# Kernel tuning notes

Measured on AMD Instinct MI355X. Metric: run time of the kernel, lower is better.

## Reference

```python
import jax, jax.numpy as jnp
import numpy as np

NUM_HEADS = 16
ROPE_THETA = 10000.0


def _rope_cos_sin(head_dim, seq_len, theta=ROPE_THETA):
    # matches precompute_freqs_cis: theta ** (-(2i)/head_dim)
    exps = -(jnp.arange(0, head_dim, 2)[: head_dim // 2].astype(jnp.float32)) / head_dim
    freqs = theta ** exps                                   # [hd/2]
    ang = jnp.arange(seq_len, dtype=jnp.float32)[:, None] * freqs[None, :]  # [S, hd/2]
    return jnp.cos(ang), jnp.sin(ang)


def _apply_rope(x, cos, sin):
    # x: [B, H, S, hd]; interpret consecutive pairs as complex numbers
    x2 = x.reshape(*x.shape[:-1], -1, 2)
    xr, xi = x2[..., 0], x2[..., 1]
    c = cos[None, None]  # [1,1,S,hd/2]
    s = sin[None, None]
    outr = xr * c - xi * s
    outi = xr * s + xi * c
    return jnp.stack([outr, outi], axis=-1).reshape(x.shape)


def setup_inputs() -> dict:
    key = jax.random.key(0)
    ks = jax.random.split(key, 9)
    B, S, D = 2, 2048, 1024
    scale = 0.02
    x = jax.random.normal(ks[0], (B, S, D), jnp.float32)
    Wq = jax.random.normal(ks[1], (D, D), jnp.float32) * scale
    bq = jax.random.normal(ks[2], (D,), jnp.float32) * scale
    Wk = jax.random.normal(ks[3], (D, D), jnp.float32) * scale
    bk = jax.random.normal(ks[4], (D,), jnp.float32) * scale
    Wv = jax.random.normal(ks[5], (D, D), jnp.float32) * scale
    bv = jax.random.normal(ks[6], (D,), jnp.float32) * scale
    Wo = jax.random.normal(ks[7], (D, D), jnp.float32) * scale
    return {"x": x, "Wq": Wq, "bq": bq, "Wk": Wk, "bk": bk,
            "Wv": Wv, "bv": bv, "Wo": Wo}


def reference(x, Wq, bq, Wk, bk, Wv, bv, Wo):
    B, S, D = x.shape
    H = NUM_HEADS
    hd = D // H
    # projections (torch Linear: x @ W.T + b), split heads -> [B,H,S,hd]
    q = (x @ Wq.T + bq).reshape(B, S, H, hd).transpose(0, 2, 1, 3)
    k = (x @ Wk.T + bk).reshape(B, S, H, hd).transpose(0, 2, 1, 3)
    v = (x @ Wv.T + bv).reshape(B, S, H, hd).transpose(0, 2, 1, 3)
    cos, sin = _rope_cos_sin(hd, S)
    q = _apply_rope(q, cos, sin)
    k = _apply_rope(k, cos, sin)
    # NOTE: original scales by sqrt(input_dim), not sqrt(head_dim)
    inv_scale = 1.0 / jnp.sqrt(jnp.asarray(D, jnp.float32))
    scores = jax.nn.softmax(jnp.einsum('bhqd,bhkd->bhqk', q, k) * inv_scale, axis=-1)
    out = jnp.einsum('bhqk,bhkd->bhqd', scores, v)
    out = out.transpose(0, 2, 1, 3).reshape(B, S, D)
    return out @ Wo.T
```

## Files before the change

### kernel.cpp

```cpp
#include <hip/hip_runtime.h>
#include <math.h>

namespace {
constexpr int kB = 2;
constexpr int kS = 2048;
constexpr int kD = 1024;
constexpr int kH = 16;
constexpr int kHD = 64;
constexpr int kBS = kB * kS;
constexpr float kInvScale = 0.03125f;
constexpr int BM = 128, BN = 64, BK = 64;
}

typedef __attribute__((ext_vector_type(8))) short short8;
typedef __attribute__((ext_vector_type(4))) float f32x4;
typedef __attribute__((ext_vector_type(4))) unsigned short u16x4;
typedef __attribute__((ext_vector_type(4))) unsigned int u32x4;

__device__ inline unsigned short f2bf(float f) {
  union { float f; unsigned u; } v;
  v.f = f;
  unsigned r = v.u + 0x7FFFu + ((v.u >> 16) & 1u);
  return (unsigned short)(r >> 16);
}

__device__ inline unsigned pack_bf16_pair(float lo, float hi) {
  union { float f; unsigned u; } a, b;
  a.f = hi; b.f = lo;
  return __builtin_amdgcn_perm(a.u + 0x8000u, b.u + 0x8000u, 0x07060302u);
}

__device__ inline void gload_lds16(const unsigned short* g, unsigned short* l) {
  __builtin_amdgcn_global_load_lds(
      (const __attribute__((address_space(1))) void*)g,
      (__attribute__((address_space(3))) void*)l, 16, 0, 0);
}

__global__ __launch_bounds__(256) void cast_prep_kernel(
    const float* __restrict__ x, const float* __restrict__ Wq,
    const float* __restrict__ Wk, const float* __restrict__ Wv,
    const float* __restrict__ Wo, unsigned short* __restrict__ xb,
    unsigned short* __restrict__ wb, float2* __restrict__ rope) {
  const int tid = blockIdx.x * 256 + threadIdx.x;
  const int stride = gridDim.x * 256;
  for (int i = tid; i < 1048576; i += stride) {
    const float* src;
    unsigned short* dst;
    int off;
    if (i < 524288) {
      src = x; dst = xb; off = i;
    } else {
      const int j = i - 524288;
      const int w = j >> 17;
      src = (w == 0) ? Wq : (w == 1) ? Wk : (w == 2) ? Wv : Wo;
      dst = wb + (size_t)w * (kD * kD);
      off = j & 131071;
    }
    const float4 a = reinterpret_cast<const float4*>(src)[off * 2];
    const float4 b = reinterpret_cast<const float4*>(src)[off * 2 + 1];
    short8 o;
    o[0] = (short)f2bf(a.x); o[1] = (short)f2bf(a.y);
    o[2] = (short)f2bf(a.z); o[3] = (short)f2bf(a.w);
    o[4] = (short)f2bf(b.x); o[5] = (short)f2bf(b.y);
    o[6] = (short)f2bf(b.z); o[7] = (short)f2bf(b.w);
    reinterpret_cast<short8*>(dst)[off] = o;
  }
  for (int i = tid; i < kS * 32; i += stride) {
    const int s = i >> 5;
    const int pr = i & 31;
    const float f = powf(10000.0f, -(float)pr / 32.0f);
    const float ang = (float)s * f;
    rope[i] = make_float2(cosf(ang), sinf(ang));
  }
}

__global__ __launch_bounds__(256) void gemm_bt_kernel(
    const unsigned short* __restrict__ A, const unsigned short* __restrict__ Wb,
    const float* __restrict__ bq, const float* __restrict__ bk,
    const float* __restrict__ bv, const float2* __restrict__ rope,
    unsigned short* __restrict__ qo, unsigned short* __restrict__ ko,
    unsigned short* __restrict__ vo, float* __restrict__ outp, int mode_base) {
  const int mode = mode_base + blockIdx.z;
  const unsigned short* __restrict__ W = Wb + (size_t)mode * (kD * kD);
  const int rt = blockIdx.x * BM;
  const int ct = blockIdx.y * BN;
  const int t = threadIdx.x;
  const int wv = t >> 6;
  const int lane = t & 63;
  const int l15 = lane & 15;
  const int lg = lane >> 4;
  const int wr = wv >> 1;
  const int wc = wv & 1;

  __shared__ unsigned short As[BM * BK];
  __shared__ unsigned short Bs[BN * BK];

  f32x4 acc[4][2];
#pragma unroll
  for (int m = 0; m < 4; ++m)
#pragma unroll
    for (int n = 0; n < 2; ++n) acc[m][n] = f32x4{0.f, 0.f, 0.f, 0.f};

  for (int kt = 0; kt < kD / BK; ++kt) {
    const int k0 = kt * BK;
    __syncthreads();
#pragma unroll
    for (int i = 0; i < 4; ++i) {
      const int off = wv * 4096 + i * 1024;
      const int p = off + lane * 16;
      const int row = p >> 7;
      const int src = ((p >> 4) & 7) ^ (row & 7);
      gload_lds16(A + (size_t)(rt + row) * kD + k0 + src * 8, As + off / 2);
    }
#pragma unroll
    for (int i = 0; i < 2; ++i) {
      const int off = wv * 2048 + i * 1024;
      const int p = off + lane * 16;
      const int row = p >> 7;
      const int src = ((p >> 4) & 7) ^ (row & 7);
      gload_lds16(W + (size_t)(ct + row) * kD + k0 + src * 8, Bs + off / 2);
    }
    __syncthreads();

#pragma unroll
    for (int ks = 0; ks < 2; ++ks) {
      short8 af[4], bf[2];
#pragma unroll
      for (int m = 0; m < 4; ++m) {
        const int row = wr * 64 + m * 16 + l15;
        const int chunk = (ks * 4 + lg) ^ (row & 7);
        af[m] = *reinterpret_cast<const short8*>(&As[row * BK + chunk * 8]);
      }
#pragma unroll
      for (int n = 0; n < 2; ++n) {
        const int row = wc * 32 + n * 16 + l15;
        const int chunk = (ks * 4 + lg) ^ (row & 7);
        bf[n] = *reinterpret_cast<const short8*>(&Bs[row * BK + chunk * 8]);
      }
      __builtin_amdgcn_s_setprio(1);
#pragma unroll
      for (int m = 0; m < 4; ++m)
#pragma unroll
        for (int n = 0; n < 2; ++n)
          acc[m][n] = __builtin_amdgcn_mfma_f32_16x16x32_bf16(
              af[m], bf[n], acc[m][n], 0, 0, 0);
      __builtin_amdgcn_s_setprio(0);
    }
  }

#pragma unroll
  for (int m = 0; m < 4; ++m) {
    const int grow0 = rt + wr * 64 + m * 16 + lg * 4;
    const int bb = grow0 >> 11;
    const int s0 = grow0 & (kS - 1);
#pragma unroll
    for (int n = 0; n < 2; ++n) {
      const int gcol = ct + wc * 32 + n * 16 + l15;
      if (mode == 3) {
#pragma unroll
        for (int reg = 0; reg < 4; ++reg)
          outp[(size_t)(grow0 + reg) * kD + gcol] = acc[m][n][reg];
      } else if (mode == 2) {
        const float bsv = bv[gcol];
        const int h = gcol >> 6, d = gcol & 63;
        u16x4 o;
#pragma unroll
        for (int reg = 0; reg < 4; ++reg)
          o[reg] = f2bf(acc[m][n][reg] + bsv);
        *reinterpret_cast<u16x4*>(
            &vo[((size_t)(bb * kH + h) * kHD + d) * kS + s0]) = o;
      } else {
        const float bsv = (mode == 0) ? bq[gcol] : bk[gcol];
        const float post = (mode == 0) ? kInvScale : 1.0f;
        unsigned short* __restrict__ dst = (mode == 0) ? qo : ko;
        const int h = gcol >> 6, d = gcol & 63;
        const int pr = d >> 1;
        const float sgn = (d & 1) ? 1.0f : -1.0f;
#pragma unroll
        for (int reg = 0; reg < 4; ++reg) {
          const int s = s0 + reg;
          const float val = acc[m][n][reg] + bsv;
          const float par = __shfl_xor(val, 1);
          const float2 cs = rope[s * 32 + pr];
          const float o = (val * cs.x + par * cs.y * sgn) * post;
          dst[((size_t)(bb * kH + h) * kS + s) * kHD + d] = f2bf(o);
        }
      }
    }
  }
}

__global__ __launch_bounds__(512) void attn_mfma_kernel(
    const unsigned short* __restrict__ qb, const unsigned short* __restrict__ kb,
    const unsigned short* __restrict__ vtb, unsigned short* __restrict__ attn) {
  const int qt = blockIdx.x;
  const int h = blockIdx.y;
  const int b = blockIdx.z;
  const int t = threadIdx.x;
  const int wave = t >> 6;
  const int lane = t & 63;
  const int l15 = lane & 15;
  const int lg = lane >> 4;
  const int g = wave >> 2;
  const int st = wave & 3;

  __shared__ __align__(16) unsigned char smem[2 * 8192 + 2 * 8192 + 512];
  unsigned short* Ks0 = (unsigned short*)smem;
  unsigned short* Vs0 = (unsigned short*)(smem + 16384);
  float* Ocomb = (float*)smem;
  float* lcomb = (float*)(smem + 32768);

  const size_t bh = (size_t)(b * kH + h);
  const unsigned short* qp = qb + bh * kS * kHD;
  const unsigned short* kp = kb + bh * kS * kHD;
  const unsigned short* vp = vtb + bh * (size_t)kHD * kS;

  const int qrow0 = qt * 128 + st * 32;

  short8 qf[2][2];
#pragma unroll
  for (int qi = 0; qi < 2; ++qi)
#pragma unroll
    for (int f = 0; f < 2; ++f)
      qf[qi][f] = *reinterpret_cast<const short8*>(
          qp + (size_t)(qrow0 + qi * 16 + l15) * kHD + f * 32 + lg * 8);

  short8 ones;
#pragma unroll
  for (int j = 0; j < 8; ++j) ones[j] = (short)0x3F80;

  f32x4 acc_o[2][4], acc_l[2];
#pragma unroll
  for (int qi = 0; qi < 2; ++qi) {
    acc_l[qi] = f32x4{0.f, 0.f, 0.f, 0.f};
#pragma unroll
    for (int ot = 0; ot < 4; ++ot) acc_o[qi][ot] = f32x4{0.f, 0.f, 0.f, 0.f};
  }

  const int srow = t >> 3;
  const int sc = (t & 7) ^ (srow & 7);
  const int kvrow = (srow & 0x23) | ((srow & 0x0C) << 1) | ((srow & 0x10) >> 2);
  const int ldsoff = wave * 512;

  gload_lds16(kp + (size_t)kvrow * kHD + sc * 8, &Ks0[ldsoff]);
  gload_lds16(vp + (size_t)srow * kS + sc * 8, &Vs0[ldsoff]);
  __syncthreads();

  constexpr int NT = kS / 64;
  for (int kt = 0; kt < NT; ++kt) {
    const int cur = kt & 1;
    unsigned short* Ksc = Ks0 + cur * 4096;
    unsigned short* Vsc = Vs0 + cur * 4096;
    if (kt + 1 < NT) {
      gload_lds16(kp + (size_t)((kt + 1) * 64 + kvrow) * kHD + sc * 8,
                  &Ks0[(cur ^ 1) * 4096 + ldsoff]);
      gload_lds16(vp + (size_t)srow * kS + (kt + 1) * 64 + sc * 8,
                  &Vs0[(cur ^ 1) * 4096 + ldsoff]);
    }

    short8 kf[2][2], vf[4];
#pragma unroll
    for (int nt = 0; nt < 2; ++nt) {
      const int row = g * 32 + nt * 16 + l15;
#pragma unroll
      for (int f = 0; f < 2; ++f) {
        const int c = (f * 4 + lg) ^ (row & 7);
        kf[nt][f] = *reinterpret_cast<const short8*>(&Ksc[row * 64 + c * 8]);
      }
    }
#pragma unroll
    for (int ot = 0; ot < 4; ++ot) {
      const int row = ot * 16 + l15;
      const int c = (4 * g + lg) ^ (row & 7);
      vf[ot] = *reinterpret_cast<const short8*>(&Vsc[row * 64 + c * 8]);
    }

    f32x4 acc_s[2][2];
    __builtin_amdgcn_s_setprio(1);
#pragma unroll
    for (int qi = 0; qi < 2; ++qi)
#pragma unroll
      for (int nt = 0; nt < 2; ++nt) {
        acc_s[qi][nt] = __builtin_amdgcn_mfma_f32_16x16x32_bf16(
            kf[nt][0], qf[qi][0], f32x4{0.f, 0.f, 0.f, 0.f}, 0, 0, 0);
        acc_s[qi][nt] = __builtin_amdgcn_mfma_f32_16x16x32_bf16(
            kf[nt][1], qf[qi][1], acc_s[qi][nt], 0, 0, 0);
      }
    __builtin_amdgcn_s_setprio(0);

#pragma unroll
    for (int qi = 0; qi < 2; ++qi) {
      float p[2][4];
#pragma unroll
      for (int nt = 0; nt < 2; ++nt)
#pragma unroll
        for (int r = 0; r < 4; ++r) p[nt][r] = __expf(acc_s[qi][nt][r]);

      short8 pb;
      {
        u32x4 w;
        w.x = pack_bf16_pair(p[0][0], p[0][1]);
        w.y = pack_bf16_pair(p[0][2], p[0][3]);
        w.z = pack_bf16_pair(p[1][0], p[1][1]);
        w.w = pack_bf16_pair(p[1][2], p[1][3]);
        pb = *reinterpret_cast<short8*>(&w);
      }

      __builtin_amdgcn_s_setprio(1);
#pragma unroll
      for (int ot = 0; ot < 4; ++ot)
        acc_o[qi][ot] = __builtin_amdgcn_mfma_f32_16x16x32_bf16(
            vf[ot], pb, acc_o[qi][ot], 0, 0, 0);
      acc_l[qi] = __builtin_amdgcn_mfma_f32_16x16x32_bf16(
          ones, pb, acc_l[qi], 0, 0, 0);
      __builtin_amdgcn_s_setprio(0);
    }

    __syncthreads();
  }

  if (g == 1) {
#pragma unroll
    for (int qi = 0; qi < 2; ++qi) {
      const int row = qi * 16 + l15;
#pragma unroll
      for (int ot = 0; ot < 4; ++ot)
        *reinterpret_cast<f32x4*>(
            &Ocomb[(st * 32 + row) * 64 + ot * 16 + lg * 4]) = acc_o[qi][ot];
      if (lg == 0) lcomb[st * 32 + row] = acc_l[qi][0];
    }
  }
  __syncthreads();
  if (g == 0) {
#pragma unroll
    for (int qi = 0; qi < 2; ++qi) {
      const int row = qi * 16 + l15;
      const float l = acc_l[qi][0] + lcomb[st * 32 + row];
      const float inv_l = 1.0f / l;
      const int s = qrow0 + row;
      unsigned short* __restrict__ dst =
          attn + ((size_t)b * kS + s) * kD + h * kHD;
#pragma unroll
      for (int ot = 0; ot < 4; ++ot) {
        const f32x4 oth = *reinterpret_cast<const f32x4*>(
            &Ocomb[(st * 32 + row) * 64 + ot * 16 + lg * 4]);
        u16x4 o;
        o[0] = f2bf((acc_o[qi][ot][0] + oth[0]) * inv_l);
        o[1] = f2bf((acc_o[qi][ot][1] + oth[1]) * inv_l);
        o[2] = f2bf((acc_o[qi][ot][2] + oth[2]) * inv_l);
        o[3] = f2bf((acc_o[qi][ot][3] + oth[3]) * inv_l);
        *reinterpret_cast<u16x4*>(&dst[ot * 16 + lg * 4]) = o;
      }
    }
  }
}

extern "C" void kernel_launch(void* const* d_in, const int* in_sizes, int n_in,
                              void* d_out, int out_size, void* d_ws,
                              size_t ws_size, hipStream_t stream) {
  (void)in_sizes; (void)n_in; (void)out_size; (void)ws_size;
  const float* x = (const float*)d_in[0];
  const float* Wq = (const float*)d_in[1];
  const float* bq = (const float*)d_in[2];
  const float* Wk = (const float*)d_in[3];
  const float* bk = (const float*)d_in[4];
  const float* Wv = (const float*)d_in[5];
  const float* bv = (const float*)d_in[6];
  const float* Wo = (const float*)d_in[7];
  float* out = (float*)d_out;

  const size_t n = (size_t)kBS * kD;
  float2* rope = (float2*)d_ws;
  unsigned short* xb = (unsigned short*)(rope + kS * 32);
  unsigned short* wb = xb + n;
  unsigned short* qb = wb + 4 * (size_t)kD * kD;
  unsigned short* kb = qb + n;
  unsigned short* vt = kb + n;
  unsigned short* attnb = vt + n;

  cast_prep_kernel<<<2048, 256, 0, stream>>>(x, Wq, Wk, Wv, Wo, xb, wb, rope);

  dim3 gq(kBS / BM, kD / BN, 3);
  gemm_bt_kernel<<<gq, dim3(256), 0, stream>>>(xb, wb, bq, bk, bv, rope, qb,
                                               kb, vt, nullptr, 0);

  dim3 ga(kS / 128, kH, kB);
  attn_mfma_kernel<<<ga, dim3(512), 0, stream>>>(qb, kb, vt, attnb);

  dim3 go(kBS / BM, kD / BN, 1);
  gemm_bt_kernel<<<go, dim3(256), 0, stream>>>(attnb, wb, bq, bk, bv, rope, qb,
                                               kb, vt, out, 3);
}
```

Baseline: 107.3 us.

## Triple-buffer K/V tiles with vmcnt waits and fold log2e into Q scale

The attention loop moves from double to triple buffering of K/V tiles in LDS, issuing loads two tiles ahead. It replaces the full __syncthreads with a partial s_waitcnt vmcnt plus a raw barrier, so one tile's loads can stay in flight across the barrier. Separately, log2(e) is folded into the Q projection scale so the softmax can use the hardware exp2 instead of __expf. This raises LDS use per block, which may lower occupancy, and depends on the manual vmcnt accounting being correct.

```diff
diff --git a/kernel.cpp b/kernel.cpp
--- a/kernel.cpp
+++ b/kernel.cpp
@@ -9,6 +9,7 @@
 constexpr int kHD = 64;
 constexpr int kBS = kB * kS;
 constexpr float kInvScale = 0.03125f;
+constexpr float kQScale = 0.03125f * 1.4426950408889634f;
 constexpr int BM = 128, BN = 64, BK = 64;
 }
 
@@ -171,7 +172,7 @@
             &vo[((size_t)(bb * kH + h) * kHD + d) * kS + s0]) = o;
       } else {
         const float bsv = (mode == 0) ? bq[gcol] : bk[gcol];
-        const float post = (mode == 0) ? kInvScale : 1.0f;
+        const float post = (mode == 0) ? kQScale : 1.0f;
         unsigned short* __restrict__ dst = (mode == 0) ? qo : ko;
         const int h = gcol >> 6, d = gcol & 63;
         const int pr = d >> 1;
@@ -204,11 +205,11 @@
   const int g = wave >> 2;
   const int st = wave & 3;
 
-  __shared__ __align__(16) unsigned char smem[2 * 8192 + 2 * 8192 + 512];
+  __shared__ __align__(16) unsigned char smem[3 * 8192 * 2 + 512];
   unsigned short* Ks0 = (unsigned short*)smem;
-  unsigned short* Vs0 = (unsigned short*)(smem + 16384);
+  unsigned short* Vs0 = (unsigned short*)(smem + 24576);
   float* Ocomb = (float*)smem;
-  float* lcomb = (float*)(smem + 32768);
+  float* lcomb = (float*)(smem + 49152);
 
   const size_t bh = (size_t)(b * kH + h);
   const unsigned short* qp = qb + bh * kS * kHD;
@@ -244,19 +245,24 @@
 
   gload_lds16(kp + (size_t)kvrow * kHD + sc * 8, &Ks0[ldsoff]);
   gload_lds16(vp + (size_t)srow * kS + sc * 8, &Vs0[ldsoff]);
-  __syncthreads();
+  gload_lds16(kp + (size_t)(64 + kvrow) * kHD + sc * 8, &Ks0[4096 + ldsoff]);
+  gload_lds16(vp + (size_t)srow * kS + 64 + sc * 8, &Vs0[4096 + ldsoff]);
+  asm volatile("s_waitcnt vmcnt(2)" ::: "memory");
+  __builtin_amdgcn_s_barrier();
 
   constexpr int NT = kS / 64;
+  int cur = 0, nxt2 = 2;
   for (int kt = 0; kt < NT; ++kt) {
-    const int cur = kt & 1;
+    if (kt + 2 < NT) {
+      const int nb = (kt + 2) * 64;
+      gload_lds16(kp + (size_t)(nb + kvrow) * kHD + sc * 8,
+                  &Ks0[nxt2 * 4096 + ldsoff]);
+      gload_lds16(vp + (size_t)srow * kS + nb + sc * 8,
+                  &Vs0[nxt2 * 4096 + ldsoff]);
+    }
+
     unsigned short* Ksc = Ks0 + cur * 4096;
     unsigned short* Vsc = Vs0 + cur * 4096;
-    if (kt + 1 < NT) {
-      gload_lds16(kp + (size_t)((kt + 1) * 64 + kvrow) * kHD + sc * 8,
-                  &Ks0[(cur ^ 1) * 4096 + ldsoff]);
-      gload_lds16(vp + (size_t)srow * kS + (kt + 1) * 64 + sc * 8,
-                  &Vs0[(cur ^ 1) * 4096 + ldsoff]);
-    }
 
     short8 kf[2][2], vf[4];
 #pragma unroll
@@ -294,7 +300,8 @@
 #pragma unroll
       for (int nt = 0; nt < 2; ++nt)
 #pragma unroll
-        for (int r = 0; r < 4; ++r) p[nt][r] = __expf(acc_s[qi][nt][r]);
+        for (int r = 0; r < 4; ++r)
+          p[nt][r] = __builtin_amdgcn_exp2f(acc_s[qi][nt][r]);
 
       short8 pb;
       {
@@ -316,8 +323,18 @@
       __builtin_amdgcn_s_setprio(0);
     }
 
-    __syncthreads();
-  }
+    if (kt < NT - 1) {
+      if (kt + 2 < NT)
+        asm volatile("s_waitcnt vmcnt(2)" ::: "memory");
+      else
+        asm volatile("s_waitcnt vmcnt(0)" ::: "memory");
+      __builtin_amdgcn_s_barrier();
+    }
+    cur = (cur == 2) ? 0 : cur + 1;
+    nxt2 = (nxt2 == 2) ? 0 : nxt2 + 1;
+  }
+
+  __syncthreads();
 
   if (g == 1) {
 #pragma unroll
```

Measured after the change: 106.0 us. About the same (-1.2%).
